# Kernel tuning notes

Measured on AMD Instinct MI355X. Metric: run time of the kernel, lower is better.

## Reference

```python
import jax, jax.numpy as jnp
import numpy as np

B, TX, TZ, DX, DZ, DATT, DMID, H, DOUT = 8, 1024, 1024, 1024, 1024, 64, 64, 16, 1024


def setup_inputs() -> dict:
    key = jax.random.key(0)
    ks = jax.random.split(key, 10)
    s = 0.02
    return {
        "x": jax.random.normal(ks[0], (B, TX, DX), jnp.float32),
        "z": jax.random.normal(ks[1], (B, TZ, DZ), jnp.float32),
        "Wq": jax.random.normal(ks[2], (H, DX, DATT), jnp.float32) * s,
        "bq": jax.random.normal(ks[3], (H, DATT), jnp.float32) * s,
        "Wk": jax.random.normal(ks[4], (H, DZ, DATT), jnp.float32) * s,
        "bk": jax.random.normal(ks[5], (H, DATT), jnp.float32) * s,
        "Wv": jax.random.normal(ks[6], (H, DZ, DMID), jnp.float32) * s,
        "bv": jax.random.normal(ks[7], (H, DMID), jnp.float32) * s,
        "Wp": jax.random.normal(ks[8], (H * DMID, DOUT), jnp.float32) * s,
        "bp": jax.random.normal(ks[9], (DOUT,), jnp.float32) * s,
        "mask": jnp.tril(jnp.ones((TX, TZ), dtype=bool)),  # causal
    }


def reference(x, z, Wq, bq, Wk, bk, Wv, bv, Wp, bp, mask):
    # Per-head projections (heads batched via stacked weights). bhxe = batch, head, x-pos, feat
    Q = jnp.einsum('bxd,hde->bhxe', x, Wq) + bq[None, :, None, :]
    K = jnp.einsum('bzd,hde->bhze', z, Wk) + bk[None, :, None, :]
    V = jnp.einsum('bzd,hde->bhze', z, Wv) + bv[None, :, None, :]
    # Scores, mask (set ~mask to -inf), then scale by 1/sqrt(Datt) (as original: mask before scale)
    S = jnp.einsum('bhxe,bhze->bhxz', Q, K)
    S = jnp.where(mask[None, None, :, :], S, -jnp.inf) * (1.0 / jnp.sqrt(jnp.asarray(DATT, S.dtype)))
    A = jax.nn.softmax(S, axis=-1)
    y = jnp.einsum('bhxz,bhze->bhxe', A, V)          # [B, H, Tx, Dmid]
    y_concat = y.transpose(0, 2, 1, 3).reshape(B, TX, H * DMID)  # concat heads
    return y_concat @ Wp + bp
```

## Files before the change

### kernel.cpp

```cpp
#include <hip/hip_runtime.h>
#include <stdint.h>


typedef float    f32x4  __attribute__((ext_vector_type(4)));
typedef __bf16   bf16x8 __attribute__((ext_vector_type(8)));
typedef unsigned short u16x4 __attribute__((ext_vector_type(4)));
typedef unsigned short u16x8 __attribute__((ext_vector_type(8)));

#define MASKNEG (-3.0e38f)
#define QSCALE_F (0.125f * 1.4426950408889634f)

__device__ __forceinline__ unsigned short f2bf(float f) {
  unsigned int u = __float_as_uint(f);
  u += 0x7fffu + ((u >> 16) & 1u);
  return (unsigned short)(u >> 16);
}

__device__ __forceinline__ void gload16(const void* g, void* s) {
  const __attribute__((address_space(1))) unsigned int* gp =
      (const __attribute__((address_space(1))) unsigned int*)(uintptr_t)g;
  __attribute__((address_space(3))) unsigned int* lp =
      (__attribute__((address_space(3))) unsigned int*)(unsigned int)(uintptr_t)s;
  __builtin_amdgcn_global_load_lds(gp, lp, 16, 0, 0);
}

__device__ __forceinline__ f32x4 mfma16(bf16x8 a, bf16x8 b, f32x4 c) {
  return __builtin_amdgcn_mfma_f32_16x16x32_bf16(a, b, c, 0, 0, 0);
}


__global__ __launch_bounds__(256) void k_cvt2(const float* __restrict__ x,
                                              const float* __restrict__ z,
                                              unsigned short* __restrict__ out) {
  int i = blockIdx.x * 256 + threadIdx.x;
  const int stride = gridDim.x * 256;
  for (; i < 2097152; i += stride) {
    const float* in = (i < 1048576) ? (x + (size_t)i * 8) : (z + (size_t)(i - 1048576) * 8);
    const f32x4* p = (const f32x4*)in;
    f32x4 a = p[0], b = p[1];
    u16x8 o;
    o[0] = f2bf(a[0]); o[1] = f2bf(a[1]); o[2] = f2bf(a[2]); o[3] = f2bf(a[3]);
    o[4] = f2bf(b[0]); o[5] = f2bf(b[1]); o[6] = f2bf(b[2]); o[7] = f2bf(b[3]);
    *(u16x8*)(out + (size_t)i * 8) = o;
  }
}

__global__ __launch_bounds__(256) void k_pack(const float* __restrict__ Wq,
                                              const float* __restrict__ Wk,
                                              const float* __restrict__ Wv,
                                              const float* __restrict__ Wp,
                                              unsigned short* __restrict__ Oq,
                                              unsigned short* __restrict__ Ok,
                                              unsigned short* __restrict__ Ov,
                                              unsigned short* __restrict__ Op) {
  __shared__ float tile[64][65];
  const int t = threadIdx.x;
  const int zid = blockIdx.z;
  if (zid < 3) {
    const float* W = zid == 0 ? Wq : (zid == 1 ? Wk : Wv);
    unsigned short* O = zid == 0 ? Oq : (zid == 1 ? Ok : Ov);
    const int h = blockIdx.x, d0 = blockIdx.y * 64;
    const int ee = t & 63, r0 = t >> 6;
#pragma unroll
    for (int dd = r0; dd < 64; dd += 4)
      tile[dd][ee] = W[(h * 1024 + d0 + dd) * 64 + ee];
    __syncthreads();
    const int d = t & 63, e0 = t >> 6;
#pragma unroll
    for (int e = e0; e < 64; e += 4)
      O[(h * 64 + e) * 1024 + d0 + d] = f2bf(tile[d][e]);
  } else {
    const int k0 = blockIdx.x * 64, n0 = blockIdx.y * 64;
    const int nn = t & 63, r0 = t >> 6;
#pragma unroll
    for (int kk = r0; kk < 64; kk += 4)
      tile[kk][nn] = Wp[(k0 + kk) * 1024 + n0 + nn];
    __syncthreads();
    const int kk = t & 63, e0 = t >> 6;
#pragma unroll
    for (int n2 = e0; n2 < 64; n2 += 4)
      Op[(n0 + n2) * 1024 + k0 + kk] = f2bf(tile[kk][n2]);
  }
}

__device__ __forceinline__ void gemm_body(const unsigned short* __restrict__ A,
                                          const unsigned short* __restrict__ Bt,
                                          const float* __restrict__ bias,
                                          void* __restrict__ outp,
                                          int mode, float oscale,
                                          int brow, int bcol,
                                          unsigned short* As, unsigned short* Bs) {
  const int tid = threadIdx.x;
  const int l = tid & 63, w = tid >> 6;
  const int lrow = l & 15, lk = l >> 4;
  const int wr = (w >> 1) * 128, wc = (w & 1) * 64;

  const int arow = tid >> 2;
  const int asrc = ((tid & 3) ^ ((arow >> 1) & 3)) * 8;
  const unsigned short* ag0 = A + (size_t)(brow + arow) * 1024 + asrc;
  const unsigned short* bg0 = Bt + (size_t)(bcol + arow) * 1024 + asrc;

  int aoff[8], boff[4];
#pragma unroll
  for (int m = 0; m < 8; m++) {
    int row = wr + m * 16 + lrow;
    aoff[m] = row * 64 + ((lk ^ ((row >> 1) & 3)) << 4);
  }
#pragma unroll
  for (int n = 0; n < 4; n++) {
    int col = wc + n * 16 + lrow;
    boff[n] = col * 64 + ((lk ^ ((col >> 1) & 3)) << 4);
  }

  f32x4 acc[8][4];
#pragma unroll
  for (int n = 0; n < 4; n++) {
    float bv = bias[bcol + wc + n * 16 + lrow];
#pragma unroll
    for (int m = 0; m < 8; m++) acc[m][n] = (f32x4){bv, bv, bv, bv};
  }

#define STAGE_G(kt, slot)                                                  \
  {                                                                        \
    char* asb = (char*)As + (slot) * 16384 + w * 1024;                     \
    char* bsb = (char*)Bs + (slot) * 8192 + w * 1024;                      \
    gload16(ag0 + (kt) * 32,          asb);                                \
    gload16(ag0 + (kt) * 32 + 65536,  asb + 4096);                         \
    gload16(ag0 + (kt) * 32 + 131072, asb + 8192);                         \
    gload16(ag0 + (kt) * 32 + 196608, asb + 12288);                        \
    gload16(bg0 + (kt) * 32,          bsb);                                \
    gload16(bg0 + (kt) * 32 + 65536,  bsb + 4096);                         \
  }

  STAGE_G(0, 0)
  STAGE_G(1, 1)
  asm volatile("s_waitcnt vmcnt(6)" ::: "memory");
  __builtin_amdgcn_s_barrier();
  __builtin_amdgcn_sched_barrier(0);

  int s0 = 0, s2 = 2;
#pragma unroll 1
  for (int kt = 0; kt < 32; kt++) {
    if (kt < 30) STAGE_G(kt + 2, s2)
    const char* ab = (const char*)As + s0 * 16384;
    const char* bb = (const char*)Bs + s0 * 8192;
    bf16x8 bfr[4];
#pragma unroll
    for (int n = 0; n < 4; n++) bfr[n] = *(const bf16x8*)(bb + boff[n]);
#pragma unroll
    for (int m = 0; m < 8; m++) {
      bf16x8 af = *(const bf16x8*)(ab + aoff[m]);
#pragma unroll
      for (int n = 0; n < 4; n++)
        acc[m][n] = mfma16(af, bfr[n], acc[m][n]);
    }
    if (kt < 31) {
      if (kt < 30) {
        asm volatile("s_waitcnt vmcnt(6)" ::: "memory");
      } else {
        asm volatile("s_waitcnt vmcnt(0)" ::: "memory");
      }
      __builtin_amdgcn_s_barrier();
      __builtin_amdgcn_sched_barrier(0);
    }
    s0 = (s0 == 2) ? 0 : s0 + 1;
    s2 = (s2 == 2) ? 0 : s2 + 1;
  }
#undef STAGE_G

  if (mode == 0) {
    unsigned short* C = (unsigned short*)outp;
#pragma unroll
    for (int m = 0; m < 8; m++) {
      int r = brow + wr + m * 16 + 4 * lk;
#pragma unroll
      for (int n = 0; n < 4; n++) {
        int c = bcol + wc + n * 16 + lrow;
        unsigned short* p = C + ((r >> 10) * 16 + (c >> 6)) * 65536 + (r & 1023) * 64 + (c & 63);
#pragma unroll
        for (int j = 0; j < 4; j++) p[j * 64] = f2bf(acc[m][n][j] * oscale);
      }
    }
  } else if (mode == 2) {
    unsigned short* C = (unsigned short*)outp;
#pragma unroll
    for (int m = 0; m < 8; m++) {
      int r = brow + wr + m * 16 + 4 * lk;
#pragma unroll
      for (int n = 0; n < 4; n++) {
        int c = bcol + wc + n * 16 + lrow;
        u16x4 o;
#pragma unroll
        for (int j = 0; j < 4; j++) o[j] = f2bf(acc[m][n][j]);
        *(u16x4*)(C + ((r >> 10) * 16 + (c >> 6)) * 65536 + (c & 63) * 1024 + (r & 1023)) = o;
      }
    }
  } else {
    float* C = (float*)outp;
#pragma unroll
    for (int m = 0; m < 8; m++) {
      int r = brow + wr + m * 16 + 4 * lk;
#pragma unroll
      for (int n = 0; n < 4; n++) {
        int c = bcol + wc + n * 16 + lrow;
#pragma unroll
        for (int j = 0; j < 4; j++) C[(r + j) * 1024 + c] = acc[m][n][j];
      }
    }
  }
}

__global__ __launch_bounds__(256, 2) void k_gemm_qkv(const unsigned short* __restrict__ Xb,
                                                     const unsigned short* __restrict__ Zb,
                                                     const unsigned short* __restrict__ Wqkv,
                                                     const float* __restrict__ bq,
                                                     const float* __restrict__ bk,
                                                     const float* __restrict__ bv,
                                                     unsigned short* __restrict__ Qp,
                                                     unsigned short* __restrict__ Kp,
                                                     unsigned short* __restrict__ Vtp) {
  __shared__ unsigned short As[24576];
  __shared__ unsigned short Bs[12288];
  const int brow = blockIdx.x * 256;
  const int cg = blockIdx.y;
  const int seg = cg >> 3;
  const int bcol = (cg & 7) * 128;
  const unsigned short* A = (seg == 0) ? Xb : Zb;
  const unsigned short* Bt = Wqkv + (size_t)seg * 1048576;
  const float* bias = (seg == 0) ? bq : (seg == 1 ? bk : bv);
  void* outp = (seg == 0) ? (void*)Qp : (seg == 1 ? (void*)Kp : (void*)Vtp);
  const int mode = (seg == 2) ? 2 : 0;
  const float oscale = (seg == 0) ? QSCALE_F : 1.0f;
  gemm_body(A, Bt, bias, outp, mode, oscale, brow, bcol, As, Bs);
}

__global__ __launch_bounds__(256, 2) void k_gemm(const unsigned short* __restrict__ A,
                                                 const unsigned short* __restrict__ Bt,
                                                 const float* __restrict__ bias,
                                                 void* __restrict__ outp,
                                                 int mode, float oscale) {
  __shared__ unsigned short As[24576];
  __shared__ unsigned short Bs[12288];
  gemm_body(A, Bt, bias, outp, mode, oscale, blockIdx.x * 256, blockIdx.y * 128, As, Bs);
}

__global__ __launch_bounds__(256, 2) void k_attn(const unsigned short* __restrict__ Qh,
                                                 const unsigned short* __restrict__ Kh,
                                                 const unsigned short* __restrict__ Vth,
                                                 unsigned short* __restrict__ Y) {
  __shared__ unsigned short Ks[16384];
  __shared__ unsigned short Vs[16384];
  __shared__ unsigned short Ps[8192];

  const int tid = threadIdx.x, l = tid & 63, w = tid >> 6;
  const int lrow = l & 15, lk = l >> 4;
  const int bh = blockIdx.y;
  const int pp = blockIdx.x;

  const unsigned short* Qb = Qh + bh * 65536;
  const unsigned short* Kb = Kh + bh * 65536;
  const unsigned short* Vb = Vth + bh * 65536;

  bf16x8 ones;
#pragma unroll
  for (int j = 0; j < 8; j++) ones[j] = (__bf16)1.0f;

  const int krl = l >> 3;
  const int kgp = l & 7;
  const unsigned short* kgsrc = Kb + (w * 32 + krl) * 64 + ((kgp ^ krl) * 8);
  const int vrl = l >> 4;
  const int vgp = l & 15;
  const int vr0 = w * 16 + 0 * 4 + vrl;
  const int vr1 = w * 16 + 1 * 4 + vrl;
  const int vr2 = w * 16 + 2 * 4 + vrl;
  const int vr3 = w * 16 + 3 * 4 + vrl;
  const int voff0 = vr0 * 1024 + ((vgp ^ (vr0 & 15)) * 8);
  const int voff1 = vr1 * 1024 + ((vgp ^ (vr1 & 15)) * 8);
  const int voff2 = vr2 * 1024 + ((vgp ^ (vr2 & 15)) * 8);
  const int voff3 = vr3 * 1024 + ((vgp ^ (vr3 & 15)) * 8);

  char* pw = (char*)Ps + w * 4096;

  const int b = bh >> 4, h = bh & 15;

#pragma unroll 1
  for (int hp = 0; hp < 2; hp++) {
    const int qi = hp == 0 ? (7 - pp) : pp;
    const int qw = qi * 128 + w * 32;
    const int qmax = qw + 31;

    bf16x8 qf[2][2];
#pragma unroll
    for (int qn = 0; qn < 2; qn++) {
      const unsigned short* qp = Qb + (qw + qn * 16 + lrow) * 64 + lk * 8;
      qf[qn][0] = *(const bf16x8*)qp;
      qf[qn][1] = *(const bf16x8*)(qp + 32);
    }

    f32x4 m[2], lsum[2], yacc[2][4];
#pragma unroll
    for (int qn = 0; qn < 2; qn++) {
      m[qn] = (f32x4){MASKNEG, MASKNEG, MASKNEG, MASKNEG};
      lsum[qn] = (f32x4){0.f, 0.f, 0.f, 0.f};
#pragma unroll
      for (int ef = 0; ef < 4; ef++) yacc[qn][ef] = (f32x4){0.f, 0.f, 0.f, 0.f};
    }

    const int nt = qi + 1;

    {
      char* kb = (char*)Ks + w * 4096;
      char* vb2 = (char*)Vs + w * 4096;
      gload16(kgsrc + 0,    kb);
      gload16(kgsrc + 512,  kb + 1024);
      gload16(kgsrc + 1024, kb + 2048);
      gload16(kgsrc + 1536, kb + 3072);
      gload16(Vb + voff0, vb2);
      gload16(Vb + voff1, vb2 + 1024);
      gload16(Vb + voff2, vb2 + 2048);
      gload16(Vb + voff3, vb2 + 3072);
    }
    __syncthreads();

#pragma unroll 1
    for (int t = 0; t < nt; t++) {
      const int z0 = t * 128;
      const int cur = t & 1;
      if (t < nt - 1) {
        const int zn = (t + 1) * 128;
        char* kb = (char*)Ks + (cur ^ 1) * 16384 + w * 4096;
        char* vb2 = (char*)Vs + (cur ^ 1) * 16384 + w * 4096;
        const unsigned short* kgt = kgsrc + zn * 64;
        gload16(kgt + 0,    kb);
        gload16(kgt + 512,  kb + 1024);
        gload16(kgt + 1024, kb + 2048);
        gload16(kgt + 1536, kb + 3072);
        gload16(Vb + voff0 + zn, vb2);
        gload16(Vb + voff1 + zn, vb2 + 1024);
        gload16(Vb + voff2 + zn, vb2 + 2048);
        gload16(Vb + voff3 + zn, vb2 + 3072);
      }

      if (z0 <= qmax) {
        const char* kbase = (const char*)Ks + cur * 16384;
        const char* vbase = (const char*)Vs + cur * 16384;

        f32x4 s[2][8];
#pragma unroll
        for (int qn = 0; qn < 2; qn++)
#pragma unroll
          for (int zf = 0; zf < 8; zf++) s[qn][zf] = (f32x4){0.f, 0.f, 0.f, 0.f};
#pragma unroll
        for (int zf = 0; zf < 8; zf++) {
          int zr = zf * 16 + lrow;
#pragma unroll
          for (int kf = 0; kf < 2; kf++) {
            bf16x8 kfr = *(const bf16x8*)(kbase + zr * 128 + (((kf * 4 + lk) ^ (zr & 7)) << 4));
            s[0][zf] = mfma16(qf[0][kf], kfr, s[0][zf]);
            s[1][zf] = mfma16(qf[1][kf], kfr, s[1][zf]);
          }
        }

        if (z0 + 127 > qw) {
#pragma unroll
          for (int qn = 0; qn < 2; qn++) {
            int qbase = qw + qn * 16 + 4 * lk;
#pragma unroll
            for (int zf = 0; zf < 8; zf++) {
              int zg = z0 + zf * 16 + lrow;
#pragma unroll
              for (int j = 0; j < 4; j++)
                if (zg > qbase + j) s[qn][zf][j] = MASKNEG;
            }
          }
        }

#pragma unroll
        for (int qn = 0; qn < 2; qn++) {
          f32x4 rm4 = s[qn][0];
#pragma unroll
          for (int zf = 1; zf < 8; zf++)
#pragma unroll
            for (int j = 0; j < 4; j++) rm4[j] = fmaxf(rm4[j], s[qn][zf][j]);
#pragma unroll
          for (int j = 0; j < 4; j++) {
            float r = rm4[j];
            r = fmaxf(r, __shfl_xor(r, 1));
            r = fmaxf(r, __shfl_xor(r, 2));
            r = fmaxf(r, __shfl_xor(r, 4));
            r = fmaxf(r, __shfl_xor(r, 8));
            rm4[j] = r;
          }
          int trig = (rm4[0] > m[qn][0] + 8.f) | (rm4[1] > m[qn][1] + 8.f) |
                     (rm4[2] > m[qn][2] + 8.f) | (rm4[3] > m[qn][3] + 8.f);
          if (__any(trig)) {
#pragma unroll
            for (int j = 0; j < 4; j++) {
              float mn = fmaxf(m[qn][j], rm4[j]);
              float a = __builtin_amdgcn_exp2f(m[qn][j] - mn);
              m[qn][j] = mn;
              lsum[qn][j] *= a;
#pragma unroll
              for (int ef = 0; ef < 4; ef++) yacc[qn][ef][j] *= a;
            }
          }
#pragma unroll
          for (int zf = 0; zf < 8; zf++)
#pragma unroll
            for (int j = 0; j < 4; j++)
              s[qn][zf][j] = __builtin_amdgcn_exp2f(s[qn][zf][j] - m[qn][j]);
        }

#pragma unroll
        for (int hf = 0; hf < 2; hf++) {
          if (z0 + hf * 64 <= qmax) {
#pragma unroll
            for (int qn = 0; qn < 2; qn++) {
#pragma unroll
              for (int zf2 = 0; zf2 < 4; zf2++) {
                int zfg = hf * 4 + zf2;
                int zc = zf2 * 16 + lrow;
                int zp = zc >> 3;
#pragma unroll
                for (int j = 0; j < 4; j++) {
                  int q = 4 * lk + j;
                  *(unsigned short*)(pw + (qn * 16 + q) * 128 + ((zp ^ (q & 7)) << 4) + (zc & 7) * 2)
                      = f2bf(s[qn][zfg][j]);
                }
              }
            }

            asm volatile("s_waitcnt lgkmcnt(0)" ::: "memory");
            __builtin_amdgcn_sched_barrier(0);

            bf16x8 pf[2][2];
#pragma unroll
            for (int qn = 0; qn < 2; qn++)
#pragma unroll
              for (int kf = 0; kf < 2; kf++)
                pf[qn][kf] = *(const bf16x8*)(pw + (qn * 16 + lrow) * 128 + (((kf * 4 + lk) ^ (lrow & 7)) << 4));

#pragma unroll
            for (int qn = 0; qn < 2; qn++)
#pragma unroll
              for (int kf = 0; kf < 2; kf++)
                lsum[qn] = mfma16(pf[qn][kf], ones, lsum[qn]);

#pragma unroll
            for (int ef = 0; ef < 4; ef++) {
              int er = ef * 16 + lrow;
#pragma unroll
              for (int kf = 0; kf < 2; kf++) {
                int g = hf * 8 + kf * 4 + lk;
                bf16x8 vf = *(const bf16x8*)(vbase + er * 256 + ((g ^ (er & 15)) << 4));
                yacc[0][ef] = mfma16(pf[0][kf], vf, yacc[0][ef]);
                yacc[1][ef] = mfma16(pf[1][kf], vf, yacc[1][ef]);
              }
            }
          }
        }
      }

      __syncthreads();
    }

#pragma unroll
    for (int qn = 0; qn < 2; qn++) {
      f32x4 rinv;
#pragma unroll
      for (int j = 0; j < 4; j++) rinv[j] = 1.0f / lsum[qn][j];
#pragma unroll
      for (int ef = 0; ef < 4; ef++) {
        int col = h * 64 + ef * 16 + lrow;
#pragma unroll
        for (int j = 0; j < 4; j++) {
          int x = qw + qn * 16 + lk * 4 + j;
          Y[(b * 1024 + x) * 1024 + col] = f2bf(yacc[qn][ef][j] * rinv[j]);
        }
      }
    }
  }
}

extern "C" void kernel_launch(void* const* d_in, const int* in_sizes, int n_in,
                              void* d_out, int out_size, void* d_ws, size_t ws_size,
                              hipStream_t stream) {
  const float* x  = (const float*)d_in[0];
  const float* z  = (const float*)d_in[1];
  const float* Wq = (const float*)d_in[2];
  const float* bq = (const float*)d_in[3];
  const float* Wk = (const float*)d_in[4];
  const float* bk = (const float*)d_in[5];
  const float* Wv = (const float*)d_in[6];
  const float* bv = (const float*)d_in[7];
  const float* Wp = (const float*)d_in[8];
  const float* bp = (const float*)d_in[9];
  (void)in_sizes; (void)n_in; (void)out_size; (void)ws_size;

  char* ws = (char*)d_ws;
  unsigned short* Xb  = (unsigned short*)(ws + 0);
  unsigned short* Zb  = (unsigned short*)(ws + 16777216);
  unsigned short* Wqt = (unsigned short*)(ws + 33554432);
  unsigned short* Wkt = (unsigned short*)(ws + 35651584);
  unsigned short* Wvt = (unsigned short*)(ws + 37748736);
  unsigned short* Wpt = (unsigned short*)(ws + 39845888);
  unsigned short* Qp  = (unsigned short*)(ws + 41943040);
  unsigned short* Kp  = (unsigned short*)(ws + 58720256);
  unsigned short* Vtp = (unsigned short*)(ws + 75497472);

  k_cvt2<<<dim3(2048), dim3(256), 0, stream>>>(x, z, Xb);
  k_pack<<<dim3(16, 16, 4), dim3(256), 0, stream>>>(Wq, Wk, Wv, Wp, Wqt, Wkt, Wvt, Wpt);

  k_gemm_qkv<<<dim3(32, 24), dim3(256), 0, stream>>>(Xb, Zb, Wqt, bq, bk, bv, Qp, Kp, Vtp);

  k_attn<<<dim3(4, 128), dim3(256), 0, stream>>>(Qp, Kp, Vtp, Xb );

  k_gemm<<<dim3(32, 8), dim3(256), 0, stream>>>(Xb, Wpt, bp, d_out, 3, 1.0f);
}
```

Measured before the change: 157.8 us.

## Restructure GEMM to 128x128 tiles with double-buffered BK=64 and split-phase barriers

Result: no change. 156.8 us (-0.7%).

```diff
diff --git a/kernel.cpp b/kernel.cpp
--- a/kernel.cpp
+++ b/kernel.cpp
@@ -93,85 +93,123 @@
   const int tid = threadIdx.x;
   const int l = tid & 63, w = tid >> 6;
   const int lrow = l & 15, lk = l >> 4;
-  const int wr = (w >> 1) * 128, wc = (w & 1) * 64;
-
-  const int arow = tid >> 2;
-  const int asrc = ((tid & 3) ^ ((arow >> 1) & 3)) * 8;
-  const unsigned short* ag0 = A + (size_t)(brow + arow) * 1024 + asrc;
-  const unsigned short* bg0 = Bt + (size_t)(bcol + arow) * 1024 + asrc;
-
-  int aoff[8], boff[4];
-#pragma unroll
-  for (int m = 0; m < 8; m++) {
+  const int wr = (w >> 1) * 64, wc = (w & 1) * 64;
+
+  const int gsrc = ((l & 3) ^ ((l >> 3) & 3)) * 8;
+  const int srow = (l >> 2);
+  const unsigned short* agp0 = A + (size_t)(brow + w * 16 + srow) * 1024 + gsrc;
+  const unsigned short* agp1 = agp0 + (size_t)64 * 1024;
+  const unsigned short* bgp0 = Bt + (size_t)(bcol + w * 16 + srow) * 1024 + gsrc;
+  const unsigned short* bgp1 = bgp0 + (size_t)64 * 1024;
+
+  int aoff[4], boff[4];
+#pragma unroll
+  for (int m = 0; m < 4; m++) {
     int row = wr + m * 16 + lrow;
-    aoff[m] = row * 64 + ((lk ^ ((row >> 1) & 3)) << 4);
+    aoff[m] = row * 64 + ((lk ^ ((lrow >> 1) & 3)) << 4);
   }
 #pragma unroll
   for (int n = 0; n < 4; n++) {
     int col = wc + n * 16 + lrow;
-    boff[n] = col * 64 + ((lk ^ ((col >> 1) & 3)) << 4);
-  }
-
-  f32x4 acc[8][4];
+    boff[n] = col * 64 + ((lk ^ ((lrow >> 1) & 3)) << 4);
+  }
+
+  f32x4 acc[4][4];
 #pragma unroll
   for (int n = 0; n < 4; n++) {
     float bv = bias[bcol + wc + n * 16 + lrow];
 #pragma unroll
-    for (int m = 0; m < 8; m++) acc[m][n] = (f32x4){bv, bv, bv, bv};
-  }
-
-#define STAGE_G(kt, slot)                                                  \
+    for (int m = 0; m < 4; m++) acc[m][n] = (f32x4){bv, bv, bv, bv};
+  }
+
+#define STAGE_KH(kt, kh, db)                                               \
   {                                                                        \
-    char* asb = (char*)As + (slot) * 16384 + w * 1024;                     \
-    char* bsb = (char*)Bs + (slot) * 8192 + w * 1024;                      \
-    gload16(ag0 + (kt) * 32,          asb);                                \
-    gload16(ag0 + (kt) * 32 + 65536,  asb + 4096);                         \
-    gload16(ag0 + (kt) * 32 + 131072, asb + 8192);                         \
-    gload16(ag0 + (kt) * 32 + 196608, asb + 12288);                        \
-    gload16(bg0 + (kt) * 32,          bsb);                                \
-    gload16(bg0 + (kt) * 32 + 65536,  bsb + 4096);                         \
-  }
-
-  STAGE_G(0, 0)
-  STAGE_G(1, 1)
-  asm volatile("s_waitcnt vmcnt(6)" ::: "memory");
-  __builtin_amdgcn_s_barrier();
-  __builtin_amdgcn_sched_barrier(0);
-
-  int s0 = 0, s2 = 2;
+    char* ab = (char*)As + (db) * 16384 + (kh) * 8192 + w * 1024;          \
+    char* bb = (char*)Bs + (db) * 16384 + (kh) * 8192 + w * 1024;          \
+    gload16(agp0 + (kt) * 64 + (kh) * 32, ab);                             \
+    gload16(agp1 + (kt) * 64 + (kh) * 32, ab + 4096);                      \
+    gload16(bgp0 + (kt) * 64 + (kh) * 32, bb);                             \
+    gload16(bgp1 + (kt) * 64 + (kh) * 32, bb + 4096);                      \
+  }
+
+  STAGE_KH(0, 0, 0)
+  STAGE_KH(0, 1, 0)
+
 #pragma unroll 1
-  for (int kt = 0; kt < 32; kt++) {
-    if (kt < 30) STAGE_G(kt + 2, s2)
-    const char* ab = (const char*)As + s0 * 16384;
-    const char* bb = (const char*)Bs + s0 * 8192;
-    bf16x8 bfr[4];
-#pragma unroll
-    for (int n = 0; n < 4; n++) bfr[n] = *(const bf16x8*)(bb + boff[n]);
-#pragma unroll
-    for (int m = 0; m < 8; m++) {
-      bf16x8 af = *(const bf16x8*)(ab + aoff[m]);
-#pragma unroll
-      for (int n = 0; n < 4; n++)
-        acc[m][n] = mfma16(af, bfr[n], acc[m][n]);
-    }
-    if (kt < 31) {
-      if (kt < 30) {
-        asm volatile("s_waitcnt vmcnt(6)" ::: "memory");
-      } else {
-        asm volatile("s_waitcnt vmcnt(0)" ::: "memory");
-      }
-      __builtin_amdgcn_s_barrier();
-      __builtin_amdgcn_sched_barrier(0);
-    }
-    s0 = (s0 == 2) ? 0 : s0 + 1;
-    s2 = (s2 == 2) ? 0 : s2 + 1;
-  }
-#undef STAGE_G
+  for (int kt = 0; kt < 16; kt++) {
+    const int db = kt & 1;
+    const char* abase = (const char*)As + db * 16384;
+    const char* bbase = (const char*)Bs + db * 16384;
+    bf16x8 afr[4], bfr[2];
+
+    asm volatile("s_waitcnt vmcnt(4)" ::: "memory");
+    __builtin_amdgcn_s_barrier();
+    __builtin_amdgcn_sched_barrier(0);
+#pragma unroll
+    for (int m = 0; m < 4; m++) afr[m] = *(const bf16x8*)(abase + aoff[m]);
+    bfr[0] = *(const bf16x8*)(bbase + boff[0]);
+    bfr[1] = *(const bf16x8*)(bbase + boff[1]);
+    if (kt < 15) STAGE_KH(kt + 1, 0, db ^ 1)
+    __builtin_amdgcn_s_setprio(1);
+#pragma unroll
+    for (int m = 0; m < 4; m++) {
+      acc[m][0] = mfma16(afr[m], bfr[0], acc[m][0]);
+      acc[m][1] = mfma16(afr[m], bfr[1], acc[m][1]);
+    }
+    __builtin_amdgcn_s_setprio(0);
+
+    asm volatile("" ::: "memory");
+    __builtin_amdgcn_s_barrier();
+    __builtin_amdgcn_sched_barrier(0);
+    bfr[0] = *(const bf16x8*)(bbase + boff[2]);
+    bfr[1] = *(const bf16x8*)(bbase + boff[3]);
+    __builtin_amdgcn_s_setprio(1);
+#pragma unroll
+    for (int m = 0; m < 4; m++) {
+      acc[m][2] = mfma16(afr[m], bfr[0], acc[m][2]);
+      acc[m][3] = mfma16(afr[m], bfr[1], acc[m][3]);
+    }
+    __builtin_amdgcn_s_setprio(0);
+
+    if (kt < 15) {
+      asm volatile("s_waitcnt vmcnt(4)" ::: "memory");
+    } else {
+      asm volatile("s_waitcnt vmcnt(0)" ::: "memory");
+    }
+    __builtin_amdgcn_s_barrier();
+    __builtin_amdgcn_sched_barrier(0);
+#pragma unroll
+    for (int m = 0; m < 4; m++) afr[m] = *(const bf16x8*)(abase + 8192 + aoff[m]);
+    bfr[0] = *(const bf16x8*)(bbase + 8192 + boff[0]);
+    bfr[1] = *(const bf16x8*)(bbase + 8192 + boff[1]);
+    if (kt < 15) STAGE_KH(kt + 1, 1, db ^ 1)
+    __builtin_amdgcn_s_setprio(1);
+#pragma unroll
+    for (int m = 0; m < 4; m++) {
+      acc[m][0] = mfma16(afr[m], bfr[0], acc[m][0]);
+      acc[m][1] = mfma16(afr[m], bfr[1], acc[m][1]);
+    }
+    __builtin_amdgcn_s_setprio(0);
+
+    asm volatile("" ::: "memory");
+    __builtin_amdgcn_s_barrier();
+    __builtin_amdgcn_sched_barrier(0);
+    bfr[0] = *(const bf16x8*)(bbase + 8192 + boff[2]);
+    bfr[1] = *(const bf16x8*)(bbase + 8192 + boff[3]);
+    __builtin_amdgcn_s_setprio(1);
+#pragma unroll
+    for (int m = 0; m < 4; m++) {
+      acc[m][2] = mfma16(afr[m], bfr[0], acc[m][2]);
+      acc[m][3] = mfma16(afr[m], bfr[1], acc[m][3]);
+    }
+    __builtin_amdgcn_s_setprio(0);
+  }
+#undef STAGE_KH
 
   if (mode == 0) {
     unsigned short* C = (unsigned short*)outp;
 #pragma unroll
-    for (int m = 0; m < 8; m++) {
+    for (int m = 0; m < 4; m++) {
       int r = brow + wr + m * 16 + 4 * lk;
 #pragma unroll
       for (int n = 0; n < 4; n++) {
@@ -184,7 +222,7 @@
   } else if (mode == 2) {
     unsigned short* C = (unsigned short*)outp;
 #pragma unroll
-    for (int m = 0; m < 8; m++) {
+    for (int m = 0; m < 4; m++) {
       int r = brow + wr + m * 16 + 4 * lk;
 #pragma unroll
       for (int n = 0; n < 4; n++) {
@@ -198,7 +236,7 @@
   } else {
     float* C = (float*)outp;
 #pragma unroll
-    for (int m = 0; m < 8; m++) {
+    for (int m = 0; m < 4; m++) {
       int r = brow + wr + m * 16 + 4 * lk;
 #pragma unroll
       for (int n = 0; n < 4; n++) {
@@ -219,9 +257,9 @@
                                                      unsigned short* __restrict__ Qp,
                                                      unsigned short* __restrict__ Kp,
                                                      unsigned short* __restrict__ Vtp) {
-  __shared__ unsigned short As[24576];
-  __shared__ unsigned short Bs[12288];
-  const int brow = blockIdx.x * 256;
+  __shared__ unsigned short As[16384];
+  __shared__ unsigned short Bs[16384];
+  const int brow = blockIdx.x * 128;
   const int cg = blockIdx.y;
   const int seg = cg >> 3;
   const int bcol = (cg & 7) * 128;
@@ -239,9 +277,9 @@
                                                  const float* __restrict__ bias,
                                                  void* __restrict__ outp,
                                                  int mode, float oscale) {
-  __shared__ unsigned short As[24576];
-  __shared__ unsigned short Bs[12288];
-  gemm_body(A, Bt, bias, outp, mode, oscale, blockIdx.x * 256, blockIdx.y * 128, As, Bs);
+  __shared__ unsigned short As[16384];
+  __shared__ unsigned short Bs[16384];
+  gemm_body(A, Bt, bias, outp, mode, oscale, blockIdx.x * 128, blockIdx.y * 128, As, Bs);
 }
 
 __global__ __launch_bounds__(256, 2) void k_attn(const unsigned short* __restrict__ Qh,
@@ -511,9 +549,9 @@
   k_cvt2<<<dim3(2048), dim3(256), 0, stream>>>(x, z, Xb);
   k_pack<<<dim3(16, 16, 4), dim3(256), 0, stream>>>(Wq, Wk, Wv, Wp, Wqt, Wkt, Wvt, Wpt);
 
-  k_gemm_qkv<<<dim3(32, 24), dim3(256), 0, stream>>>(Xb, Zb, Wqt, bq, bk, bv, Qp, Kp, Vtp);
+  k_gemm_qkv<<<dim3(64, 24), dim3(256), 0, stream>>>(Xb, Zb, Wqt, bq, bk, bv, Qp, Kp, Vtp);
 
   k_attn<<<dim3(4, 128), dim3(256), 0, stream>>>(Qp, Kp, Vtp, Xb );
 
-  k_gemm<<<dim3(32, 8), dim3(256), 0, stream>>>(Xb, Wpt, bp, d_out, 3, 1.0f);
-}
+  k_gemm<<<dim3(64, 8), dim3(256), 0, stream>>>(Xb, Wpt, bp, d_out, 3, 1.0f);
+}
```

## Transpose QK^T MFMA so each lane owns one query row

Applied to the files above, without the earlier changes.

Result: faster. 151.8 us (-3.8%).

```diff
diff --git a/kernel.cpp b/kernel.cpp
--- a/kernel.cpp
+++ b/kernel.cpp
@@ -297,10 +297,11 @@
       qf[qn][1] = *(const bf16x8*)(qp + 32);
     }
 
-    f32x4 m[2], lsum[2], yacc[2][4];
+    float mm[2];
+    f32x4 lsum[2], yacc[2][4];
 #pragma unroll
     for (int qn = 0; qn < 2; qn++) {
-      m[qn] = (f32x4){MASKNEG, MASKNEG, MASKNEG, MASKNEG};
+      mm[qn] = MASKNEG;
       lsum[qn] = (f32x4){0.f, 0.f, 0.f, 0.f};
 #pragma unroll
       for (int ef = 0; ef < 4; ef++) yacc[qn][ef] = (f32x4){0.f, 0.f, 0.f, 0.f};
@@ -356,59 +357,54 @@
 #pragma unroll
           for (int kf = 0; kf < 2; kf++) {
             bf16x8 kfr = *(const bf16x8*)(kbase + zr * 128 + (((kf * 4 + lk) ^ (zr & 7)) << 4));
-            s[0][zf] = mfma16(qf[0][kf], kfr, s[0][zf]);
-            s[1][zf] = mfma16(qf[1][kf], kfr, s[1][zf]);
+            s[0][zf] = mfma16(kfr, qf[0][kf], s[0][zf]);
+            s[1][zf] = mfma16(kfr, qf[1][kf], s[1][zf]);
           }
         }
 
         if (z0 + 127 > qw) {
 #pragma unroll
           for (int qn = 0; qn < 2; qn++) {
-            int qbase = qw + qn * 16 + 4 * lk;
+            int qg = qw + qn * 16 + lrow;
 #pragma unroll
             for (int zf = 0; zf < 8; zf++) {
-              int zg = z0 + zf * 16 + lrow;
+              int zb = z0 + zf * 16 + 4 * lk;
 #pragma unroll
               for (int j = 0; j < 4; j++)
-                if (zg > qbase + j) s[qn][zf][j] = MASKNEG;
+                if (zb + j > qg) s[qn][zf][j] = MASKNEG;
             }
           }
         }
 
 #pragma unroll
         for (int qn = 0; qn < 2; qn++) {
-          f32x4 rm4 = s[qn][0];
+          f32x4 r4 = s[qn][0];
 #pragma unroll
           for (int zf = 1; zf < 8; zf++)
 #pragma unroll
-            for (int j = 0; j < 4; j++) rm4[j] = fmaxf(rm4[j], s[qn][zf][j]);
-#pragma unroll
-          for (int j = 0; j < 4; j++) {
-            float r = rm4[j];
-            r = fmaxf(r, __shfl_xor(r, 1));
-            r = fmaxf(r, __shfl_xor(r, 2));
-            r = fmaxf(r, __shfl_xor(r, 4));
-            r = fmaxf(r, __shfl_xor(r, 8));
-            rm4[j] = r;
+            for (int j = 0; j < 4; j++) r4[j] = fmaxf(r4[j], s[qn][zf][j]);
+          float rm = fmaxf(fmaxf(r4[0], r4[1]), fmaxf(r4[2], r4[3]));
+          rm = fmaxf(rm, __shfl_xor(rm, 16));
+          rm = fmaxf(rm, __shfl_xor(rm, 32));
+
+          if (__any(rm > mm[qn] + 8.f)) {
+            float mn = fmaxf(mm[qn], rm);
+            float a = __builtin_amdgcn_exp2f(mm[qn] - mn);
+            mm[qn] = mn;
+            f32x4 av;
+#pragma unroll
+            for (int j = 0; j < 4; j++)
+              av[j] = __shfl(a, (l & 48) | (lk * 4 + j));
+            lsum[qn] *= av;
+#pragma unroll
+            for (int ef = 0; ef < 4; ef++) yacc[qn][ef] *= av;
           }
-          int trig = (rm4[0] > m[qn][0] + 8.f) | (rm4[1] > m[qn][1] + 8.f) |
-                     (rm4[2] > m[qn][2] + 8.f) | (rm4[3] > m[qn][3] + 8.f);
-          if (__any(trig)) {
-#pragma unroll
-            for (int j = 0; j < 4; j++) {
-              float mn = fmaxf(m[qn][j], rm4[j]);
-              float a = __builtin_amdgcn_exp2f(m[qn][j] - mn);
-              m[qn][j] = mn;
-              lsum[qn][j] *= a;
-#pragma unroll
-              for (int ef = 0; ef < 4; ef++) yacc[qn][ef][j] *= a;
-            }
-          }
+          float mk = mm[qn];
 #pragma unroll
           for (int zf = 0; zf < 8; zf++)
 #pragma unroll
             for (int j = 0; j < 4; j++)
-              s[qn][zf][j] = __builtin_amdgcn_exp2f(s[qn][zf][j] - m[qn][j]);
+              s[qn][zf][j] = __builtin_amdgcn_exp2f(s[qn][zf][j] - mk);
         }
 
 #pragma unroll
@@ -416,17 +412,16 @@
           if (z0 + hf * 64 <= qmax) {
 #pragma unroll
             for (int qn = 0; qn < 2; qn++) {
+              int q = qn * 16 + lrow;
+              char* rowp = pw + q * 128;
 #pragma unroll
               for (int zf2 = 0; zf2 < 4; zf2++) {
                 int zfg = hf * 4 + zf2;
-                int zc = zf2 * 16 + lrow;
-                int zp = zc >> 3;
-#pragma unroll
-                for (int j = 0; j < 4; j++) {
-                  int q = 4 * lk + j;
-                  *(unsigned short*)(pw + (qn * 16 + q) * 128 + ((zp ^ (q & 7)) << 4) + (zc & 7) * 2)
-                      = f2bf(s[qn][zfg][j]);
-                }
+                u16x4 o;
+#pragma unroll
+                for (int j = 0; j < 4; j++) o[j] = f2bf(s[qn][zfg][j]);
+                int g = zf2 * 2 + (lk >> 1);
+                *(u16x4*)(rowp + ((g ^ (q & 7)) << 4) + (lk & 1) * 8) = o;
               }
             }
 
```
